# Optimization experiments

Hardware: AMD Instinct MI355X
Metric: run time of the kernel (lower is better)

## Reference

```python
import jax, jax.numpy as jnp
import numpy as np

N_NODES = 50000
BN_EPS = 1e-5
L2_EPS = 1e-12


def setup_inputs() -> dict:
    key = jax.random.key(0)
    k_h, k_w, k_s, k_d = jax.random.split(key, 4)
    h = jax.random.normal(k_h, (N_NODES, 128), dtype=jnp.float32)
    W = jax.random.normal(k_w, (128, 128), dtype=jnp.float32) * (1.0 / np.sqrt(128))
    gamma = jnp.ones((128,), dtype=jnp.float32)
    beta = jnp.zeros((128,), dtype=jnp.float32)
    src = jax.random.randint(k_s, (600000,), 0, N_NODES, dtype=jnp.int64 if jax.config.jax_enable_x64 else jnp.int32)
    dst = jax.random.randint(k_d, (600000,), 0, N_NODES, dtype=jnp.int64 if jax.config.jax_enable_x64 else jnp.int32)
    return {"h": h, "W": W, "gamma": gamma, "beta": beta, "src": src, "dst": dst}


def reference(h, W, gamma, beta, src, dst):
    N = h.shape[0]
    ones = jnp.ones(src.shape[0], dtype=h.dtype)
    # degrees, clamped to >= 1 (DGL GraphConv norm='both')
    deg_out = jnp.clip(jax.ops.segment_sum(ones, src, num_segments=N), 1.0)
    deg_in = jnp.clip(jax.ops.segment_sum(ones, dst, num_segments=N), 1.0)
    # src-side normalization
    hn = h * jax.lax.rsqrt(deg_out)[:, None]
    # gather-scatter aggregation over edges (sum of src messages at dst)
    agg = jax.ops.segment_sum(hn[src], dst, num_segments=N)  # [N, dim_in]
    # dst-side normalization, then linear (in_feats <= out_feats branch)
    agg = agg * jax.lax.rsqrt(deg_in)[:, None]
    out = agg @ W  # [N, dim_out]
    # BatchNorm1d (training-mode batch stats, biased variance)
    mu = jnp.mean(out, axis=0)
    var = jnp.mean(jnp.square(out - mu), axis=0)
    out = (out - mu) * jax.lax.rsqrt(var + BN_EPS) * gamma + beta
    # ReLU
    out = jax.nn.relu(out)
    # F.normalize(p=2, dim=1)
    norm = jnp.sqrt(jnp.sum(jnp.square(out), axis=1, keepdims=True))
    out = out / jnp.maximum(norm, L2_EPS)
    return out
```

## Files before the change

### kernel.cpp

```cpp
#include <hip/hip_runtime.h>
#include <hip/hip_bf16.h>

#define N_NODES 50000
#define N_EDGES 600000
#define SLOTS 64
#define GEMM_BLOCKS 782
#define BUILD_BLOCKS 586
#define GATHER_BLOCKS 3125
#define RED_BLOCKS 125
#define CSTRIDE 32

#define Z_OFF        0ull
#define ESRCP_OFF    12800000ull
#define CURS_OFF     19200000ull
#define DEGO_OFF     25600000ull
#define ZERO_OFF     19200000ull
#define ZERO_BYTES   12800000ull
#define PSUM_OFF     32000000ull
#define PSQ_OFF      33600000ull
#define PS2_OFF      35200000ull
#define PQ2_OFF      35264000ull
#define SCALE_OFF    35328000ull
#define SHIFT_OFF    35328512ull
#define OUTPRE_OFF   35400000ull

typedef short bf16x8 __attribute__((ext_vector_type(8)));
typedef float f32x4  __attribute__((ext_vector_type(4)));

__device__ __forceinline__ float bf16lo(unsigned int v) { return __uint_as_float(v << 16); }
__device__ __forceinline__ float bf16hi(unsigned int v) { return __uint_as_float(v & 0xffff0000u); }
__device__ __forceinline__ unsigned int packbf16(float x, float y) {
  union { __hip_bfloat162 v; unsigned int u; } cvt;
  cvt.v.x = __float2bfloat16(x);
  cvt.v.y = __float2bfloat16(y);
  return cvt.u;
}

__device__ __forceinline__ int detect_bf16(const unsigned int* hu, int tid) {
  unsigned int u = hu[tid & 63];
  int ex = (u >> 7) & 0xFF;
  unsigned long long b = __ballot(ex >= 100 && ex <= 140);
  return __popcll(b) >= 32 ? 1 : 0;
}

__global__ __launch_bounds__(256) void k_fused(const int* __restrict__ src,
                                               const int* __restrict__ dst,
                                               int* __restrict__ cursor,
                                               int* __restrict__ dego,
                                               unsigned short* __restrict__ esrcPad,
                                               const void* __restrict__ hraw,
                                               const void* __restrict__ Wraw,
                                               __hip_bfloat16* __restrict__ Z) {
  __shared__ unsigned int lb[8192];
  int t = threadIdx.x;

  if (blockIdx.x >= GEMM_BLOCKS) {
    int e0 = (blockIdx.x - GEMM_BLOCKS) * 1024 + t * 4;
    if (e0 < N_EDGES) {
      int4 s4 = *(const int4*)&src[e0];
      int4 d4 = *(const int4*)&dst[e0];
      atomicAdd(&dego[(size_t)s4.x * CSTRIDE], 1);
      atomicAdd(&dego[(size_t)s4.y * CSTRIDE], 1);
      atomicAdd(&dego[(size_t)s4.z * CSTRIDE], 1);
      atomicAdd(&dego[(size_t)s4.w * CSTRIDE], 1);
      int sl0 = atomicAdd(&cursor[(size_t)d4.x * CSTRIDE], 1);
      int sl1 = atomicAdd(&cursor[(size_t)d4.y * CSTRIDE], 1);
      int sl2 = atomicAdd(&cursor[(size_t)d4.z * CSTRIDE], 1);
      int sl3 = atomicAdd(&cursor[(size_t)d4.w * CSTRIDE], 1);
      if (sl0 < SLOTS) esrcPad[(size_t)d4.x * SLOTS + sl0] = (unsigned short)s4.x;
      if (sl1 < SLOTS) esrcPad[(size_t)d4.y * SLOTS + sl1] = (unsigned short)s4.y;
      if (sl2 < SLOTS) esrcPad[(size_t)d4.z * SLOTS + sl2] = (unsigned short)s4.z;
      if (sl3 < SLOTS) esrcPad[(size_t)d4.w * SLOTS + sl3] = (unsigned short)s4.w;
    }
    return;
  }

  const unsigned int* hu = (const unsigned int*)hraw;
  int isbf = detect_bf16(hu, t);
  int r0 = blockIdx.x * 64;

  for (int i = t; i < 8192; i += 256) {
    int tileIdx = i >> 8;
    int rem     = i & 255;
    int ln      = rem >> 2;
    int dw      = rem & 3;
    int kb      = tileIdx & 3;
    int ct      = tileIdx >> 2;
    int q       = ln >> 4;
    int n       = ln & 15;
    int k       = kb * 32 + q * 8 + dw * 2;
    int c       = ct * 16 + n;
    unsigned int val;
    if (isbf) {
      const unsigned int* Wd = (const unsigned int*)Wraw;
      unsigned int u0 = Wd[k * 64 + (c >> 1)];
      unsigned int u1 = Wd[(k + 1) * 64 + (c >> 1)];
      unsigned int h0 = (c & 1) ? (u0 >> 16) : (u0 & 0xffffu);
      unsigned int h1 = (c & 1) ? (u1 >> 16) : (u1 & 0xffffu);
      val = h0 | (h1 << 16);
    } else {
      const float* Wf = (const float*)Wraw;
      val = packbf16(Wf[k * 128 + c], Wf[(k + 1) * 128 + c]);
    }
    lb[i] = val;
  }

  int l = t & 63;
  int w = t >> 6;
  int m = l & 15;
  int q = l >> 4;

  int rA = r0 + w * 16 + m;
  bool okA = rA < N_NODES;

  bf16x8 af[4];
  if (isbf) {
    const uint4* hd = (const uint4*)hraw;
#pragma unroll
    for (int kb = 0; kb < 4; ++kb) {
      union { uint4 u; bf16x8 v; } cv;
      cv.u = okA ? hd[(size_t)rA * 16 + kb * 4 + q] : make_uint4(0u, 0u, 0u, 0u);
      af[kb] = cv.v;
    }
  } else {
    const float4* hf = (const float4*)hraw;
#pragma unroll
    for (int kb = 0; kb < 4; ++kb) {
      union { uint4 u; bf16x8 v; } cv;
      if (okA) {
        float4 f0 = hf[(size_t)rA * 32 + kb * 8 + q * 2];
        float4 f1 = hf[(size_t)rA * 32 + kb * 8 + q * 2 + 1];
        cv.u.x = packbf16(f0.x, f0.y);
        cv.u.y = packbf16(f0.z, f0.w);
        cv.u.z = packbf16(f1.x, f1.y);
        cv.u.w = packbf16(f1.z, f1.w);
      } else {
        cv.u = make_uint4(0u, 0u, 0u, 0u);
      }
      af[kb] = cv.v;
    }
  }

  f32x4 acc[8];
#pragma unroll
  for (int ct = 0; ct < 8; ++ct) acc[ct] = (f32x4){0.f, 0.f, 0.f, 0.f};

  __syncthreads();

#pragma unroll
  for (int kb = 0; kb < 4; ++kb) {
#pragma unroll
    for (int ct = 0; ct < 8; ++ct) {
      bf16x8 bfv = *(const bf16x8*)&lb[(ct * 4 + kb) * 256 + l * 4];
      acc[ct] = __builtin_amdgcn_mfma_f32_16x16x32_bf16(af[kb], bfv, acc[ct], 0, 0, 0);
    }
  }

#pragma unroll
  for (int ct = 0; ct < 8; ++ct) {
    int col = ct * 16 + m;
#pragma unroll
    for (int reg = 0; reg < 4; ++reg) {
      int row = r0 + w * 16 + q * 4 + reg;
      if (row < N_NODES) Z[(size_t)row * 128 + col] = __float2bfloat16(acc[ct][reg]);
    }
  }
}

__global__ __launch_bounds__(256) void k_gatherZ(const unsigned int* __restrict__ Zd,
                                                 const int* __restrict__ cursor,
                                                 const int* __restrict__ dego,
                                                 const unsigned short* __restrict__ esrcPad,
                                                 unsigned int* __restrict__ outpre,
                                                 float* __restrict__ psum,
                                                 float* __restrict__ psq) {
  __shared__ float sred[4 * 128];
  int t = threadIdx.x;
  int w = t >> 6;
  int l = t & 63;
  float s1a = 0.f, s1b = 0.f, s2a = 0.f, s2b = 0.f;
#pragma unroll
  for (int i = 0; i < 4; ++i) {
    int n = blockIdx.x * 16 + w * 4 + i;
    int di = cursor[(size_t)n * CSTRIDE];
    int cnt = di < SLOTS ? di : SLOTS;
    const unsigned short* row = esrcPad + (size_t)n * SLOTS;
    float a0 = 0.f, a1 = 0.f;
    int j = 0;
    for (; j + 3 < cnt; j += 4) {
      ushort4 s4 = *(const ushort4*)&row[j];
      int i0 = s4.x, i1 = s4.y, i2 = s4.z, i3 = s4.w;
      unsigned int v0 = Zd[(size_t)i0 * 64 + l];
      unsigned int v1 = Zd[(size_t)i1 * 64 + l];
      unsigned int v2 = Zd[(size_t)i2 * 64 + l];
      unsigned int v3 = Zd[(size_t)i3 * 64 + l];
      float c0 = rsqrtf((float)max(dego[(size_t)i0 * CSTRIDE], 1));
      float c1 = rsqrtf((float)max(dego[(size_t)i1 * CSTRIDE], 1));
      float c2 = rsqrtf((float)max(dego[(size_t)i2 * CSTRIDE], 1));
      float c3 = rsqrtf((float)max(dego[(size_t)i3 * CSTRIDE], 1));
      a0 = fmaf(bf16lo(v0), c0, a0); a1 = fmaf(bf16hi(v0), c0, a1);
      a0 = fmaf(bf16lo(v1), c1, a0); a1 = fmaf(bf16hi(v1), c1, a1);
      a0 = fmaf(bf16lo(v2), c2, a0); a1 = fmaf(bf16hi(v2), c2, a1);
      a0 = fmaf(bf16lo(v3), c3, a0); a1 = fmaf(bf16hi(v3), c3, a1);
    }
    for (; j < cnt; ++j) {
      int is = row[j];
      unsigned int v = Zd[(size_t)is * 64 + l];
      float c = rsqrtf((float)max(dego[(size_t)is * CSTRIDE], 1));
      a0 = fmaf(bf16lo(v), c, a0);
      a1 = fmaf(bf16hi(v), c, a1);
    }
    float scn = rsqrtf((float)(di < 1 ? 1 : di));
    a0 *= scn; a1 *= scn;
    outpre[(size_t)n * 64 + l] = packbf16(a0, a1);
    s1a += a0; s2a += a0 * a0;
    s1b += a1; s2b += a1 * a1;
  }
  sred[w * 128 + 2 * l]     = s1a;
  sred[w * 128 + 2 * l + 1] = s1b;
  __syncthreads();
  if (t < 128) {
    float v = sred[t] + sred[128 + t] + sred[256 + t] + sred[384 + t];
    psum[(size_t)blockIdx.x * 128 + t] = v;
  }
  __syncthreads();
  sred[w * 128 + 2 * l]     = s2a;
  sred[w * 128 + 2 * l + 1] = s2b;
  __syncthreads();
  if (t < 128) {
    float v = sred[t] + sred[128 + t] + sred[256 + t] + sred[384 + t];
    psq[(size_t)blockIdx.x * 128 + t] = v;
  }
}

__global__ __launch_bounds__(256) void k_bnred(const float* __restrict__ psum,
                                               const float* __restrict__ psq,
                                               float* __restrict__ ps2,
                                               float* __restrict__ pq2) {
  __shared__ float r1[256], r2[256];
  int t = threadIdx.x;
  int c = t & 127;
  int j = t >> 7;
  int b0 = blockIdx.x * 25;
  float s1 = 0.f, s2 = 0.f;
  for (int b = b0 + j; b < b0 + 25; b += 2) {
    s1 += psum[(size_t)b * 128 + c];
    s2 += psq [(size_t)b * 128 + c];
  }
  r1[t] = s1; r2[t] = s2;
  __syncthreads();
  if (j == 0) {
    ps2[(size_t)blockIdx.x * 128 + c] = s1 + r1[c + 128];
    pq2[(size_t)blockIdx.x * 128 + c] = s2 + r2[c + 128];
  }
}

__global__ __launch_bounds__(1024) void k_bnfinal(const float* __restrict__ ps2,
                                                  const float* __restrict__ pq2,
                                                  const void* __restrict__ gamma,
                                                  const void* __restrict__ beta,
                                                  const unsigned int* __restrict__ hu,
                                                  float* __restrict__ scale,
                                                  float* __restrict__ shift) {
  __shared__ float r1[1024], r2[1024];
  int t = threadIdx.x;
  int isbf = detect_bf16(hu, t);
  int c = t & 127;
  int j = t >> 7;
  float s1 = 0.f, s2 = 0.f;
  for (int b = j; b < RED_BLOCKS; b += 8) {
    s1 += ps2[(size_t)b * 128 + c];
    s2 += pq2[(size_t)b * 128 + c];
  }
  r1[t] = s1; r2[t] = s2;
  __syncthreads();
  if (j == 0) {
#pragma unroll
    for (int jj = 1; jj < 8; ++jj) { s1 += r1[c + 128 * jj]; s2 += r2[c + 128 * jj]; }
    const float invN = 1.0f / (float)N_NODES;
    float mu  = s1 * invN;
    float var = s2 * invN - mu * mu;
    float is  = rsqrtf(var + 1e-5f);
    float g, b;
    if (isbf) {
      g = __bfloat162float(((const __hip_bfloat16*)gamma)[c]);
      b = __bfloat162float(((const __hip_bfloat16*)beta)[c]);
    } else {
      g = ((const float*)gamma)[c];
      b = ((const float*)beta)[c];
    }
    scale[c] = g * is;
    shift[c] = b - mu * g * is;
  }
}

__global__ __launch_bounds__(256) void k_rownorm(const unsigned int* __restrict__ outpre,
                                                 const float* __restrict__ scale,
                                                 const float* __restrict__ shift,
                                                 const unsigned int* __restrict__ hu,
                                                 void* __restrict__ outraw) {
  int t = threadIdx.x;
  int isbf = detect_bf16(hu, t);
  int r = blockIdx.x * 4 + (t >> 6);
  int l = t & 63;
  unsigned int xv = outpre[(size_t)r * 64 + l];
  float2 sc = *(const float2*)&scale[2 * l];
  float2 sh = *(const float2*)&shift[2 * l];
  float y0 = fmaxf(bf16lo(xv) * sc.x + sh.x, 0.f);
  float y1 = fmaxf(bf16hi(xv) * sc.y + sh.y, 0.f);
  float ss = y0 * y0 + y1 * y1;
#pragma unroll
  for (int o = 1; o < 64; o <<= 1) ss += __shfl_xor(ss, o, 64);
  float inv = 1.0f / fmaxf(sqrtf(ss), 1e-12f);
  y0 *= inv; y1 *= inv;
  if (isbf) {
    ((unsigned int*)outraw)[(size_t)r * 64 + l] = packbf16(y0, y1);
  } else {
    float2 o2; o2.x = y0; o2.y = y1;
    ((float2*)outraw)[(size_t)r * 64 + l] = o2;
  }
}

extern "C" void kernel_launch(void* const* d_in, const int* in_sizes, int n_in,
                              void* d_out, int out_size, void* d_ws, size_t ws_size,
                              hipStream_t stream) {
  const void* h     = d_in[0];
  const void* W     = d_in[1];
  const void* gamma = d_in[2];
  const void* beta  = d_in[3];
  const int*  src   = (const int*)d_in[4];
  const int*  dst   = (const int*)d_in[5];

  char* ws = (char*)d_ws;
  unsigned int* Zd        = (unsigned int*)(ws + Z_OFF);
  unsigned short* esrcPad = (unsigned short*)(ws + ESRCP_OFF);
  int*   cursor  = (int*)(ws + CURS_OFF);
  int*   dego    = (int*)(ws + DEGO_OFF);
  float* psum    = (float*)(ws + PSUM_OFF);
  float* psq     = (float*)(ws + PSQ_OFF);
  float* ps2     = (float*)(ws + PS2_OFF);
  float* pq2     = (float*)(ws + PQ2_OFF);
  float* scale   = (float*)(ws + SCALE_OFF);
  float* shift   = (float*)(ws + SHIFT_OFF);
  unsigned int* outpre = (unsigned int*)(ws + OUTPRE_OFF);

  (void)hipMemsetAsync(ws + ZERO_OFF, 0, ZERO_BYTES, stream);

  hipLaunchKernelGGL(k_fused, dim3(GEMM_BLOCKS + BUILD_BLOCKS), dim3(256), 0, stream,
                     src, dst, cursor, dego, esrcPad, h, W, (__hip_bfloat16*)Zd);
  hipLaunchKernelGGL(k_gatherZ, dim3(GATHER_BLOCKS), dim3(256), 0, stream,
                     Zd, cursor, dego, esrcPad, outpre, psum, psq);
  hipLaunchKernelGGL(k_bnred, dim3(RED_BLOCKS), dim3(256), 0, stream,
                     psum, psq, ps2, pq2);
  hipLaunchKernelGGL(k_bnfinal, dim3(1), dim3(1024), 0, stream,
                     ps2, pq2, gamma, beta, (const unsigned int*)h, scale, shift);
  hipLaunchKernelGGL(k_rownorm, dim3(N_NODES / 4), dim3(256), 0, stream,
                     outpre, scale, shift, (const unsigned int*)h, (unsigned int*)d_out);
}
```

Baseline: 206.6 us.

## Compute out-degrees via LDS histogram blocks and compact cursor/degree arrays

Out-degree counting moves from global atomics on padded counters to 16 dedicated blocks. Each block scans all source indices and builds an LDS histogram for its node range. The cursor and degree arrays drop their 32-int padding stride, so the memset shrinks from 12.8 MB to 200 KB, and edge-build blocks now handle one edge per thread. The gather kernel also merges its two shared-memory reductions into one barrier phase. The cost is that each of the 16 degree blocks reads the whole src array, and dense cursor atomics may contend more on shared cache lines.

Result: slower. 353.8 us (+71.3%).

```diff
diff --git a/kernel.cpp b/kernel.cpp
--- a/kernel.cpp
+++ b/kernel.cpp
@@ -4,25 +4,31 @@
 #define N_NODES 50000
 #define N_EDGES 600000
 #define SLOTS 64
+#define DEGO_BLOCKS 16
+#define DEGO_RANGE 3125
 #define GEMM_BLOCKS 782
-#define BUILD_BLOCKS 586
+#define BUILD_BLOCKS 2344
 #define GATHER_BLOCKS 3125
 #define RED_BLOCKS 125
-#define CSTRIDE 32
+
+#define DEGO_BASE  0
+#define GEMM_BASE  (DEGO_BLOCKS)
+#define BUILD_BASE (DEGO_BLOCKS + GEMM_BLOCKS)
+#define TOTAL_BLOCKS (BUILD_BASE + BUILD_BLOCKS)
 
 #define Z_OFF        0ull
 #define ESRCP_OFF    12800000ull
 #define CURS_OFF     19200000ull
-#define DEGO_OFF     25600000ull
+#define DEGO_OFF     19400000ull
 #define ZERO_OFF     19200000ull
-#define ZERO_BYTES   12800000ull
-#define PSUM_OFF     32000000ull
-#define PSQ_OFF      33600000ull
-#define PS2_OFF      35200000ull
-#define PQ2_OFF      35264000ull
-#define SCALE_OFF    35328000ull
-#define SHIFT_OFF    35328512ull
-#define OUTPRE_OFF   35400000ull
+#define ZERO_BYTES   200000ull
+#define PSUM_OFF     19600128ull
+#define PSQ_OFF      21200128ull
+#define PS2_OFF      22800128ull
+#define PQ2_OFF      22864128ull
+#define SCALE_OFF    22928128ull
+#define SHIFT_OFF    22928640ull
+#define OUTPRE_OFF   23000064ull
 
 typedef short bf16x8 __attribute__((ext_vector_type(8)));
 typedef float f32x4  __attribute__((ext_vector_type(4)));
@@ -54,30 +60,40 @@
   __shared__ unsigned int lb[8192];
   int t = threadIdx.x;
 
-  if (blockIdx.x >= GEMM_BLOCKS) {
-    int e0 = (blockIdx.x - GEMM_BLOCKS) * 1024 + t * 4;
-    if (e0 < N_EDGES) {
-      int4 s4 = *(const int4*)&src[e0];
-      int4 d4 = *(const int4*)&dst[e0];
-      atomicAdd(&dego[(size_t)s4.x * CSTRIDE], 1);
-      atomicAdd(&dego[(size_t)s4.y * CSTRIDE], 1);
-      atomicAdd(&dego[(size_t)s4.z * CSTRIDE], 1);
-      atomicAdd(&dego[(size_t)s4.w * CSTRIDE], 1);
-      int sl0 = atomicAdd(&cursor[(size_t)d4.x * CSTRIDE], 1);
-      int sl1 = atomicAdd(&cursor[(size_t)d4.y * CSTRIDE], 1);
-      int sl2 = atomicAdd(&cursor[(size_t)d4.z * CSTRIDE], 1);
-      int sl3 = atomicAdd(&cursor[(size_t)d4.w * CSTRIDE], 1);
-      if (sl0 < SLOTS) esrcPad[(size_t)d4.x * SLOTS + sl0] = (unsigned short)s4.x;
-      if (sl1 < SLOTS) esrcPad[(size_t)d4.y * SLOTS + sl1] = (unsigned short)s4.y;
-      if (sl2 < SLOTS) esrcPad[(size_t)d4.z * SLOTS + sl2] = (unsigned short)s4.z;
-      if (sl3 < SLOTS) esrcPad[(size_t)d4.w * SLOTS + sl3] = (unsigned short)s4.w;
-    }
+  if (blockIdx.x >= BUILD_BASE) {
+    int e = (blockIdx.x - BUILD_BASE) * 256 + t;
+    if (e < N_EDGES) {
+      int s = src[e];
+      int d = dst[e];
+      int slot = atomicAdd(&cursor[d], 1);
+      if (slot < SLOTS) esrcPad[(size_t)d * SLOTS + slot] = (unsigned short)s;
+    }
+    return;
+  }
+
+  if (blockIdx.x < GEMM_BASE) {
+    int* cnt = (int*)lb;
+    int lo = blockIdx.x * DEGO_RANGE;
+    for (int i = t; i < DEGO_RANGE; i += 256) cnt[i] = 0;
+    __syncthreads();
+    const int4* s4p = (const int4*)src;
+    int nq = N_EDGES / 4;
+    for (int i = t; i < nq; i += 256) {
+      int4 s4 = s4p[i];
+      int r0 = s4.x - lo, r1 = s4.y - lo, r2 = s4.z - lo, r3 = s4.w - lo;
+      if ((unsigned)r0 < DEGO_RANGE) atomicAdd(&cnt[r0], 1);
+      if ((unsigned)r1 < DEGO_RANGE) atomicAdd(&cnt[r1], 1);
+      if ((unsigned)r2 < DEGO_RANGE) atomicAdd(&cnt[r2], 1);
+      if ((unsigned)r3 < DEGO_RANGE) atomicAdd(&cnt[r3], 1);
+    }
+    __syncthreads();
+    for (int i = t; i < DEGO_RANGE; i += 256) dego[lo + i] = cnt[i];
     return;
   }
 
   const unsigned int* hu = (const unsigned int*)hraw;
   int isbf = detect_bf16(hu, t);
-  int r0 = blockIdx.x * 64;
+  int r0 = (blockIdx.x - GEMM_BASE) * 64;
 
   for (int i = t; i < 8192; i += 256) {
     int tileIdx = i >> 8;
@@ -174,7 +190,7 @@
                                                  unsigned int* __restrict__ outpre,
                                                  float* __restrict__ psum,
                                                  float* __restrict__ psq) {
-  __shared__ float sred[4 * 128];
+  __shared__ float sred[8 * 128];
   int t = threadIdx.x;
   int w = t >> 6;
   int l = t & 63;
@@ -182,7 +198,7 @@
 #pragma unroll
   for (int i = 0; i < 4; ++i) {
     int n = blockIdx.x * 16 + w * 4 + i;
-    int di = cursor[(size_t)n * CSTRIDE];
+    int di = cursor[n];
     int cnt = di < SLOTS ? di : SLOTS;
     const unsigned short* row = esrcPad + (size_t)n * SLOTS;
     float a0 = 0.f, a1 = 0.f;
@@ -194,10 +210,10 @@
       unsigned int v1 = Zd[(size_t)i1 * 64 + l];
       unsigned int v2 = Zd[(size_t)i2 * 64 + l];
       unsigned int v3 = Zd[(size_t)i3 * 64 + l];
-      float c0 = rsqrtf((float)max(dego[(size_t)i0 * CSTRIDE], 1));
-      float c1 = rsqrtf((float)max(dego[(size_t)i1 * CSTRIDE], 1));
-      float c2 = rsqrtf((float)max(dego[(size_t)i2 * CSTRIDE], 1));
-      float c3 = rsqrtf((float)max(dego[(size_t)i3 * CSTRIDE], 1));
+      float c0 = rsqrtf((float)max(dego[i0], 1));
+      float c1 = rsqrtf((float)max(dego[i1], 1));
+      float c2 = rsqrtf((float)max(dego[i2], 1));
+      float c3 = rsqrtf((float)max(dego[i3], 1));
       a0 = fmaf(bf16lo(v0), c0, a0); a1 = fmaf(bf16hi(v0), c0, a1);
       a0 = fmaf(bf16lo(v1), c1, a0); a1 = fmaf(bf16hi(v1), c1, a1);
       a0 = fmaf(bf16lo(v2), c2, a0); a1 = fmaf(bf16hi(v2), c2, a1);
@@ -206,7 +222,7 @@
     for (; j < cnt; ++j) {
       int is = row[j];
       unsigned int v = Zd[(size_t)is * 64 + l];
-      float c = rsqrtf((float)max(dego[(size_t)is * CSTRIDE], 1));
+      float c = rsqrtf((float)max(dego[is], 1));
       a0 = fmaf(bf16lo(v), c, a0);
       a1 = fmaf(bf16hi(v), c, a1);
     }
@@ -216,20 +232,14 @@
     s1a += a0; s2a += a0 * a0;
     s1b += a1; s2b += a1 * a1;
   }
-  sred[w * 128 + 2 * l]     = s1a;
-  sred[w * 128 + 2 * l + 1] = s1b;
+  sred[w * 128 + 2 * l]           = s1a;
+  sred[w * 128 + 2 * l + 1]       = s1b;
+  sred[512 + w * 128 + 2 * l]     = s2a;
+  sred[512 + w * 128 + 2 * l + 1] = s2b;
   __syncthreads();
   if (t < 128) {
-    float v = sred[t] + sred[128 + t] + sred[256 + t] + sred[384 + t];
-    psum[(size_t)blockIdx.x * 128 + t] = v;
-  }
-  __syncthreads();
-  sred[w * 128 + 2 * l]     = s2a;
-  sred[w * 128 + 2 * l + 1] = s2b;
-  __syncthreads();
-  if (t < 128) {
-    float v = sred[t] + sred[128 + t] + sred[256 + t] + sred[384 + t];
-    psq[(size_t)blockIdx.x * 128 + t] = v;
+    psum[(size_t)blockIdx.x * 128 + t] = sred[t] + sred[128 + t] + sred[256 + t] + sred[384 + t];
+    psq [(size_t)blockIdx.x * 128 + t] = sred[512 + t] + sred[640 + t] + sred[768 + t] + sred[896 + t];
   }
 }
 
@@ -346,7 +356,7 @@
 
   (void)hipMemsetAsync(ws + ZERO_OFF, 0, ZERO_BYTES, stream);
 
-  hipLaunchKernelGGL(k_fused, dim3(GEMM_BLOCKS + BUILD_BLOCKS), dim3(256), 0, stream,
+  hipLaunchKernelGGL(k_fused, dim3(TOTAL_BLOCKS), dim3(256), 0, stream,
                      src, dst, cursor, dego, esrcPad, h, W, (__hip_bfloat16*)Zd);
   hipLaunchKernelGGL(k_gatherZ, dim3(GATHER_BLOCKS), dim3(256), 0, stream,
                      Zd, cursor, dego, esrcPad, outpre, psum, psq);
```
